# Kernel optimization log

Hardware: AMD Instinct MI355X
Metric: run time of the kernel (lower is better)

The kernel has to match this reference:

```python
import jax, jax.numpy as jnp
import numpy as np
import math

B, SQ, SK, HID, NH = 2, 2048, 512, 1024, 16
HD = HID // NH  # head dim = 64


def setup_inputs() -> dict:
    key = jax.random.key(0)
    k1, k2, k3, k4, k5 = jax.random.split(key, 5)
    return {
        "hidden_states": jax.random.normal(k1, (B, SQ, HID), dtype=jnp.float32),
        "encoder_hidden_states": jax.random.normal(k2, (B, SK, HID), dtype=jnp.float32),
        "encoder_attention_mask": jnp.ones((B, SK), dtype=jnp.int32),
        "Wq": jax.random.normal(k3, (HID, HID), dtype=jnp.float32) * (1.0 / math.sqrt(HID)),
        "Wk": jax.random.normal(k4, (HID, HID), dtype=jnp.float32) * (1.0 / math.sqrt(HID)),
        "Wv": jax.random.normal(k5, (HID, HID), dtype=jnp.float32) * (1.0 / math.sqrt(HID)),
    }


def reference(hidden_states, encoder_hidden_states, encoder_attention_mask, Wq, Wk, Wv):
    # nn.Linear(bias=False): y = x @ W.T ; split heads -> [B, H, S, D]
    def split_heads(x, S):
        return x.reshape(x.shape[0], S, NH, HD).transpose(0, 2, 1, 3)

    q = split_heads(hidden_states @ Wq.T, SQ)            # [B,H,Sq,D]
    k = split_heads(encoder_hidden_states @ Wk.T, SK)    # [B,H,Sk,D]
    v = split_heads(encoder_hidden_states @ Wv.T, SK)    # [B,H,Sk,D]

    scores = jnp.einsum("bhqd,bhkd->bhqk", q, k) / math.sqrt(HD)  # [B,H,Sq,Sk]

    # HF-style extended mask: (1 - mask) * finfo.min, broadcast over heads/queries
    neg = jnp.finfo(scores.dtype).min
    inv_mask = (1.0 - encoder_attention_mask.astype(scores.dtype))[:, None, None, :] * neg

    probs = jax.nn.softmax(scores + inv_mask, axis=-1)
    context = jnp.einsum("bhqk,bhkd->bhqd", probs, v)    # [B,H,Sq,D]
    context = context.transpose(0, 2, 1, 3).reshape(hidden_states.shape[0], SQ, HID)
    # NOTE: returned attention_scores are scaled but UNMASKED, matching the source
    return (context, scores)
```

## Files before the change

kernel.cpp:

```cpp
#include <hip/hip_runtime.h>

#define B_   2
#define SQ_  2048
#define SK_  512
#define HID_ 1024
#define NH_  16
#define HD_  64

typedef __bf16 bf16x8 __attribute__((ext_vector_type(8)));
typedef float  f32x4  __attribute__((ext_vector_type(4)));

__device__ __forceinline__ unsigned short f2bf(float f) {
    unsigned u = __builtin_bit_cast(unsigned, f);
    u += 0x7fffu + ((u >> 16) & 1u);
    return (unsigned short)(u >> 16);
}

__device__ __forceinline__ void gll16(const unsigned short* g, unsigned short* l) {
    __builtin_amdgcn_global_load_lds(
        (const __attribute__((address_space(1))) unsigned int*)(const void*)g,
        (__attribute__((address_space(3))) unsigned int*)(void*)l,
        16, 0, 0);
}

__global__ __launch_bounds__(256) void cvt_all(const float* __restrict__ hs,
                                               const float* __restrict__ enc,
                                               const float* __restrict__ wq,
                                               const float* __restrict__ wk,
                                               const float* __restrict__ wv,
                                               unsigned short* __restrict__ hb,
                                               unsigned short* __restrict__ eb,
                                               unsigned short* __restrict__ wqb,
                                               unsigned short* __restrict__ wkb,
                                               unsigned short* __restrict__ wvb) {
    size_t i = ((size_t)blockIdx.x * 256 + threadIdx.x) * 4;
    const float* s; unsigned short* d; size_t off;
    if (i < 4194304)      { s = hs;  d = hb;  off = i; }
    else if (i < 5242880) { s = enc; d = eb;  off = i - 4194304; }
    else if (i < 6291456) { s = wq;  d = wqb; off = i - 5242880; }
    else if (i < 7340032) { s = wk;  d = wkb; off = i - 6291456; }
    else                  { s = wv;  d = wvb; off = i - 7340032; }
    float4 v = *reinterpret_cast<const float4*>(s + off);
    ushort4 o;
    o.x = f2bf(v.x); o.y = f2bf(v.y); o.z = f2bf(v.z); o.w = f2bf(v.w);
    *reinterpret_cast<ushort4*>(d + off) = o;
}

__global__ __launch_bounds__(256, 4) void gemm_qkv(const unsigned short* __restrict__ hb,
                                                   const unsigned short* __restrict__ eb,
                                                   const unsigned short* __restrict__ wq,
                                                   const unsigned short* __restrict__ wk,
                                                   const unsigned short* __restrict__ wv,
                                                   unsigned short* __restrict__ qo,
                                                   unsigned short* __restrict__ ko,
                                                   unsigned short* __restrict__ vo) {
    __shared__ unsigned short as[64 * 32];
    __shared__ unsigned short bs[128 * 32];

    int bid = blockIdx.x;
    int nb = bid & 7, ms = bid >> 3;
    const unsigned short* Ab; const unsigned short* Wb;
    int mrow, mode;
    if (ms < 64)      { mode = 0; Ab = hb; Wb = wq; mrow = ms * 64; }
    else if (ms < 80) { mode = 1; Ab = eb; Wb = wk; mrow = (ms - 64) * 64; }
    else              { mode = 2; Ab = eb; Wb = wv; mrow = (ms - 80) * 64; }
    int n0 = nb * 128;

    int tid = threadIdx.x, lane = tid & 63, w = tid >> 6;
    int quad = lane >> 4, lc = lane & 15;

    int lrow = lane >> 2;
    int chA  = (lane & 3) ^ ((lane >> 3) & 3);
    const unsigned short* agp  = Ab + (size_t)(mrow + w * 16 + lrow) * 1024 + chA * 8;
    const unsigned short* bgp0 = Wb + (size_t)(n0 + w * 32 + lrow) * 1024 + chA * 8;
    const unsigned short* bgp1 = bgp0 + (size_t)16 * 1024;
    unsigned short* asl  = &as[(w * 16) * 32];
    unsigned short* bsl0 = &bs[(w * 32) * 32];
    unsigned short* bsl1 = &bs[(w * 32 + 16) * 32];

    f32x4 zero4 = {0.f, 0.f, 0.f, 0.f};
    f32x4 acc[4][2];
#pragma unroll
    for (int i = 0; i < 4; i++) { acc[i][0] = zero4; acc[i][1] = zero4; }

    int rsw = (lc >> 1) & 3;
    for (int k0 = 0; k0 < 1024; k0 += 32) {
        gll16(agp + k0, asl);
        gll16(bgp0 + k0, bsl0);
        gll16(bgp1 + k0, bsl1);
        __syncthreads();
        bf16x8 af[4], bfr[2];
#pragma unroll
        for (int mt = 0; mt < 4; mt++)
            af[mt] = *reinterpret_cast<const bf16x8*>(&as[(mt * 16 + lc) * 32 + (quad ^ rsw) * 8]);
#pragma unroll
        for (int nt = 0; nt < 2; nt++)
            bfr[nt] = *reinterpret_cast<const bf16x8*>(&bs[(w * 32 + nt * 16 + lc) * 32 + (quad ^ rsw) * 8]);
#pragma unroll
        for (int mt = 0; mt < 4; mt++)
#pragma unroll
            for (int nt = 0; nt < 2; nt++)
                acc[mt][nt] = __builtin_amdgcn_mfma_f32_16x16x32_bf16(af[mt], bfr[nt], acc[mt][nt], 0, 0, 0);
        __syncthreads();
    }

#pragma unroll
    for (int mt = 0; mt < 4; mt++) {
#pragma unroll
        for (int nt = 0; nt < 2; nt++) {
            int n = n0 + w * 32 + nt * 16 + lc;
            int h = n >> 6, d = n & 63;
#pragma unroll
            for (int r = 0; r < 4; r++) {
                int M = mrow + mt * 16 + quad * 4 + r;
                unsigned short val = f2bf(acc[mt][nt][r]);
                if (mode == 0) {
                    int b = M >> 11, s = M & 2047;
                    qo[(((size_t)(b * NH_ + h)) * SQ_ + s) * HD_ + d] = val;
                } else if (mode == 1) {
                    int b = M >> 9, s = M & 511;
                    ko[(((size_t)(b * NH_ + h)) * SK_ + s) * HD_ + d] = val;
                } else {
                    int b = M >> 9, s = M & 511;
                    vo[(((size_t)(b * NH_ + h)) * HD_ + d) * SK_ + s] = val;
                }
            }
        }
    }
}

#define PST 72

__global__ __launch_bounds__(256, 2) void attn_kernel(const unsigned short* __restrict__ qh,
                                                      const unsigned short* __restrict__ kh,
                                                      const unsigned short* __restrict__ vh,
                                                      const int* __restrict__ maskp,
                                                      float* __restrict__ octx,
                                                      float* __restrict__ oscores) {
    __shared__ unsigned short qs[64 * 64];
    __shared__ unsigned short ks[64 * 64];
    __shared__ unsigned short vts[64 * 64];
    __shared__ unsigned short ps[64 * PST];
    __shared__ float lm[SK_];

    int bid = blockIdx.x;
    int qt = bid & 31;
    int h  = (bid >> 5) & 15;
    int b  = bid >> 9;

    int tid = threadIdx.x, lane = tid & 63, w = tid >> 6;
    int quad = lane >> 4, lc = lane & 15;
    int wrow = w * 16;

    const unsigned short* qp = qh + ((size_t)(b * NH_ + h) * SQ_ + qt * 64) * HD_;
    const unsigned short* kp = kh + ((size_t)(b * NH_ + h) * SK_) * HD_;
    const unsigned short* vp = vh + ((size_t)(b * NH_ + h) * HD_) * SK_;

    int lr  = lane >> 3;
    int chg = (lane & 7) ^ lr;

#pragma unroll
    for (int j = 0; j < 2; j++) {
        int c = w * 2 + j;
        gll16(qp + (c * 8 + lr) * 64 + chg * 8, &qs[c * 512]);
    }
#pragma unroll
    for (int i = 0; i < 2; i++) {
        int c = tid + i * 256;
        lm[c] = maskp[b * SK_ + c] ? 0.0f : -3.0e38f;
    }
    __syncthreads();

    int rsw = lc & 7;
    bf16x8 qf[2];
#pragma unroll
    for (int hf = 0; hf < 2; hf++)
        qf[hf] = *reinterpret_cast<const bf16x8*>(&qs[(wrow + lc) * 64 + ((quad + hf * 4) ^ rsw) * 8]);

    f32x4 zero4 = {0.f, 0.f, 0.f, 0.f};
    f32x4 sacc[32];
#pragma unroll
    for (int t = 0; t < 32; t++) sacc[t] = zero4;

    float* srowp = oscores + ((size_t)(b * NH_ + h) * SQ_ + qt * 64) * SK_;

    for (int kt = 0; kt < 8; kt++) {
#pragma unroll
        for (int j = 0; j < 2; j++) {
            int c = w * 2 + j;
            gll16(kp + (kt * 64 + c * 8 + lr) * 64 + chg * 8, &ks[c * 512]);
        }
        __syncthreads();
#pragma unroll
        for (int tl = 0; tl < 4; tl++) {
            int t = kt * 4 + tl;
#pragma unroll
            for (int hf = 0; hf < 2; hf++) {
                bf16x8 kf = *reinterpret_cast<const bf16x8*>(
                    &ks[(tl * 16 + lc) * 64 + ((quad + hf * 4) ^ rsw) * 8]);
                sacc[t] = __builtin_amdgcn_mfma_f32_16x16x32_bf16(kf, qf[hf], sacc[t], 0, 0, 0);
            }
        }
#pragma unroll
        for (int tl = 0; tl < 4; tl++) {
            int t = kt * 4 + tl;
            sacc[t] *= 0.125f;
            *reinterpret_cast<f32x4*>(&srowp[(size_t)(wrow + lc) * SK_ + t * 16 + quad * 4]) = sacc[t];
        }
        __syncthreads();
    }

#pragma unroll
    for (int t = 0; t < 32; t++) {
        float4 mv = *reinterpret_cast<const float4*>(&lm[t * 16 + quad * 4]);
        sacc[t][0] += mv.x; sacc[t][1] += mv.y; sacc[t][2] += mv.z; sacc[t][3] += mv.w;
    }
    float mx = -3.4e38f;
#pragma unroll
    for (int t = 0; t < 32; t++)
#pragma unroll
        for (int j = 0; j < 4; j++) mx = fmaxf(mx, sacc[t][j]);
    mx = fmaxf(mx, __shfl_xor(mx, 16));
    mx = fmaxf(mx, __shfl_xor(mx, 32));
    float sum = 0.f;
#pragma unroll
    for (int t = 0; t < 32; t++)
#pragma unroll
        for (int j = 0; j < 4; j++) {
            float e = __expf(sacc[t][j] - mx);
            sacc[t][j] = e;
            sum += e;
        }
    sum += __shfl_xor(sum, 16);
    sum += __shfl_xor(sum, 32);
    float inv = 1.0f / sum;
#pragma unroll
    for (int t = 0; t < 32; t++) sacc[t] *= inv;

    f32x4 cacc[4];
#pragma unroll
    for (int ct = 0; ct < 4; ct++) cacc[ct] = zero4;

    for (int kt = 0; kt < 8; kt++) {
#pragma unroll
        for (int tl = 0; tl < 4; tl++) {
            int t = kt * 4 + tl;
            ushort4 pk;
            pk.x = f2bf(sacc[t][0]); pk.y = f2bf(sacc[t][1]);
            pk.z = f2bf(sacc[t][2]); pk.w = f2bf(sacc[t][3]);
            *reinterpret_cast<ushort4*>(&ps[(wrow + lc) * PST + tl * 16 + quad * 4]) = pk;
        }
#pragma unroll
        for (int j = 0; j < 2; j++) {
            int c = w * 2 + j;
            gll16(vp + (size_t)(c * 8 + lr) * SK_ + kt * 64 + chg * 8, &vts[c * 512]);
        }
        __syncthreads();
#pragma unroll
        for (int ks2 = 0; ks2 < 2; ks2++) {
            bf16x8 af = *reinterpret_cast<const bf16x8*>(&ps[(wrow + lc) * PST + ks2 * 32 + quad * 8]);
#pragma unroll
            for (int ct = 0; ct < 4; ct++) {
                bf16x8 bv = *reinterpret_cast<const bf16x8*>(
                    &vts[(ct * 16 + lc) * 64 + ((quad + ks2 * 4) ^ rsw) * 8]);
                cacc[ct] = __builtin_amdgcn_mfma_f32_16x16x32_bf16(af, bv, cacc[ct], 0, 0, 0);
            }
        }
        __syncthreads();
    }

#pragma unroll
    for (int ct = 0; ct < 4; ct++) {
        int d = ct * 16 + lc;
#pragma unroll
        for (int r = 0; r < 4; r++) {
            int s = qt * 64 + wrow + quad * 4 + r;
            octx[((size_t)b * SQ_ + s) * HID_ + h * HD_ + d] = cacc[ct][r];
        }
    }
}

extern "C" void kernel_launch(void* const* d_in, const int* in_sizes, int n_in,
                              void* d_out, int out_size, void* d_ws, size_t ws_size,
                              hipStream_t stream) {
    const float* hs   = (const float*)d_in[0];
    const float* enc  = (const float*)d_in[1];
    const int*   mask = (const int*)d_in[2];
    const float* Wq   = (const float*)d_in[3];
    const float* Wk   = (const float*)d_in[4];
    const float* Wv   = (const float*)d_in[5];
    float* out = (float*)d_out;

    unsigned short* hb  = (unsigned short*)d_ws;
    unsigned short* eb  = hb  + 4194304;
    unsigned short* wqb = eb  + 1048576;
    unsigned short* wkb = wqb + 1048576;
    unsigned short* wvb = wkb + 1048576;
    unsigned short* qhp = wvb + 1048576;
    unsigned short* khp = qhp + 4194304;
    unsigned short* vhp = khp + 1048576;

    cvt_all<<<8192, 256, 0, stream>>>(hs, enc, Wq, Wk, Wv, hb, eb, wqb, wkb, wvb);
    gemm_qkv<<<768, 256, 0, stream>>>(hb, eb, wqb, wkb, wvb, qhp, khp, vhp);
    attn_kernel<<<1024, 256, 0, stream>>>(qhp, khp, vhp, mask, out, out + 4194304);
}
```

Measured before the change: 228.3 us.

## Enlarge QKV GEMM tiles to 128x128, load K/V fragments directly from global memory

The QKV GEMM now uses 128x128 output tiles with a 2x2 warp grid and 16 accumulators per wave. This halves the block count and raises operand reuse per LDS load. Both kernels remap block IDs so each group of 8 consecutive blocks touches different tiles, likely for better cache or XCD locality. The attention kernel drops its LDS staging for Q, K and V, reading MFMA fragments straight from global memory and removing the per-iteration barriers. This relies on L1/L2 reuse across waves, at the cost of uncoalesced reads and higher register pressure.

```diff
diff --git a/kernel.cpp b/kernel.cpp
--- a/kernel.cpp
+++ b/kernel.cpp
@@ -46,7 +46,7 @@
     *reinterpret_cast<ushort4*>(d + off) = o;
 }
 
-__global__ __launch_bounds__(256, 4) void gemm_qkv(const unsigned short* __restrict__ hb,
+__global__ __launch_bounds__(256, 3) void gemm_qkv(const unsigned short* __restrict__ hb,
                                                    const unsigned short* __restrict__ eb,
                                                    const unsigned short* __restrict__ wq,
                                                    const unsigned short* __restrict__ wk,
@@ -54,52 +54,61 @@
                                                    unsigned short* __restrict__ qo,
                                                    unsigned short* __restrict__ ko,
                                                    unsigned short* __restrict__ vo) {
-    __shared__ unsigned short as[64 * 32];
+    __shared__ unsigned short as[128 * 32];
     __shared__ unsigned short bs[128 * 32];
 
     int bid = blockIdx.x;
+    bid = (bid & 7) * 48 + (bid >> 3);
     int nb = bid & 7, ms = bid >> 3;
     const unsigned short* Ab; const unsigned short* Wb;
     int mrow, mode;
-    if (ms < 64)      { mode = 0; Ab = hb; Wb = wq; mrow = ms * 64; }
-    else if (ms < 80) { mode = 1; Ab = eb; Wb = wk; mrow = (ms - 64) * 64; }
-    else              { mode = 2; Ab = eb; Wb = wv; mrow = (ms - 80) * 64; }
+    if (ms < 32)      { mode = 0; Ab = hb; Wb = wq; mrow = ms * 128; }
+    else if (ms < 40) { mode = 1; Ab = eb; Wb = wk; mrow = (ms - 32) * 128; }
+    else              { mode = 2; Ab = eb; Wb = wv; mrow = (ms - 40) * 128; }
     int n0 = nb * 128;
 
     int tid = threadIdx.x, lane = tid & 63, w = tid >> 6;
     int quad = lane >> 4, lc = lane & 15;
+    int wr = w >> 1, wc = w & 1;
 
     int lrow = lane >> 2;
     int chA  = (lane & 3) ^ ((lane >> 3) & 3);
-    const unsigned short* agp  = Ab + (size_t)(mrow + w * 16 + lrow) * 1024 + chA * 8;
+    const unsigned short* agp0 = Ab + (size_t)(mrow + w * 32 + lrow) * 1024 + chA * 8;
+    const unsigned short* agp1 = agp0 + (size_t)16 * 1024;
     const unsigned short* bgp0 = Wb + (size_t)(n0 + w * 32 + lrow) * 1024 + chA * 8;
     const unsigned short* bgp1 = bgp0 + (size_t)16 * 1024;
-    unsigned short* asl  = &as[(w * 16) * 32];
+    unsigned short* asl0 = &as[(w * 32) * 32];
+    unsigned short* asl1 = &as[(w * 32 + 16) * 32];
     unsigned short* bsl0 = &bs[(w * 32) * 32];
     unsigned short* bsl1 = &bs[(w * 32 + 16) * 32];
 
     f32x4 zero4 = {0.f, 0.f, 0.f, 0.f};
-    f32x4 acc[4][2];
-#pragma unroll
-    for (int i = 0; i < 4; i++) { acc[i][0] = zero4; acc[i][1] = zero4; }
+    f32x4 acc[4][4];
+#pragma unroll
+    for (int i = 0; i < 4; i++)
+#pragma unroll
+        for (int j = 0; j < 4; j++) acc[i][j] = zero4;
 
     int rsw = (lc >> 1) & 3;
     for (int k0 = 0; k0 < 1024; k0 += 32) {
-        gll16(agp + k0, asl);
+        gll16(agp0 + k0, asl0);
+        gll16(agp1 + k0, asl1);
         gll16(bgp0 + k0, bsl0);
         gll16(bgp1 + k0, bsl1);
         __syncthreads();
-        bf16x8 af[4], bfr[2];
+        bf16x8 af[4], bfr[4];
 #pragma unroll
         for (int mt = 0; mt < 4; mt++)
-            af[mt] = *reinterpret_cast<const bf16x8*>(&as[(mt * 16 + lc) * 32 + (quad ^ rsw) * 8]);
-#pragma unroll
-        for (int nt = 0; nt < 2; nt++)
-            bfr[nt] = *reinterpret_cast<const bf16x8*>(&bs[(w * 32 + nt * 16 + lc) * 32 + (quad ^ rsw) * 8]);
+            af[mt] = *reinterpret_cast<const bf16x8*>(
+                &as[(wr * 64 + mt * 16 + lc) * 32 + (quad ^ rsw) * 8]);
+#pragma unroll
+        for (int nt = 0; nt < 4; nt++)
+            bfr[nt] = *reinterpret_cast<const bf16x8*>(
+                &bs[(wc * 64 + nt * 16 + lc) * 32 + (quad ^ rsw) * 8]);
 #pragma unroll
         for (int mt = 0; mt < 4; mt++)
 #pragma unroll
-            for (int nt = 0; nt < 2; nt++)
+            for (int nt = 0; nt < 4; nt++)
                 acc[mt][nt] = __builtin_amdgcn_mfma_f32_16x16x32_bf16(af[mt], bfr[nt], acc[mt][nt], 0, 0, 0);
         __syncthreads();
     }
@@ -107,12 +116,12 @@
 #pragma unroll
     for (int mt = 0; mt < 4; mt++) {
 #pragma unroll
-        for (int nt = 0; nt < 2; nt++) {
-            int n = n0 + w * 32 + nt * 16 + lc;
+        for (int nt = 0; nt < 4; nt++) {
+            int n = n0 + wc * 64 + nt * 16 + lc;
             int h = n >> 6, d = n & 63;
 #pragma unroll
             for (int r = 0; r < 4; r++) {
-                int M = mrow + mt * 16 + quad * 4 + r;
+                int M = mrow + wr * 64 + mt * 16 + quad * 4 + r;
                 unsigned short val = f2bf(acc[mt][nt][r]);
                 if (mode == 0) {
                     int b = M >> 11, s = M & 2047;
@@ -137,13 +146,11 @@
                                                       const int* __restrict__ maskp,
                                                       float* __restrict__ octx,
                                                       float* __restrict__ oscores) {
-    __shared__ unsigned short qs[64 * 64];
-    __shared__ unsigned short ks[64 * 64];
-    __shared__ unsigned short vts[64 * 64];
     __shared__ unsigned short ps[64 * PST];
     __shared__ float lm[SK_];
 
     int bid = blockIdx.x;
+    bid = (bid & 7) * 128 + (bid >> 3);
     int qt = bid & 31;
     int h  = (bid >> 5) & 15;
     int b  = bid >> 9;
@@ -156,14 +163,6 @@
     const unsigned short* kp = kh + ((size_t)(b * NH_ + h) * SK_) * HD_;
     const unsigned short* vp = vh + ((size_t)(b * NH_ + h) * HD_) * SK_;
 
-    int lr  = lane >> 3;
-    int chg = (lane & 7) ^ lr;
-
-#pragma unroll
-    for (int j = 0; j < 2; j++) {
-        int c = w * 2 + j;
-        gll16(qp + (c * 8 + lr) * 64 + chg * 8, &qs[c * 512]);
-    }
 #pragma unroll
     for (int i = 0; i < 2; i++) {
         int c = tid + i * 256;
@@ -171,11 +170,10 @@
     }
     __syncthreads();
 
-    int rsw = lc & 7;
     bf16x8 qf[2];
 #pragma unroll
     for (int hf = 0; hf < 2; hf++)
-        qf[hf] = *reinterpret_cast<const bf16x8*>(&qs[(wrow + lc) * 64 + ((quad + hf * 4) ^ rsw) * 8]);
+        qf[hf] = *reinterpret_cast<const bf16x8*>(qp + (wrow + lc) * 64 + hf * 32 + quad * 8);
 
     f32x4 zero4 = {0.f, 0.f, 0.f, 0.f};
     f32x4 sacc[32];
@@ -184,20 +182,15 @@
 
     float* srowp = oscores + ((size_t)(b * NH_ + h) * SQ_ + qt * 64) * SK_;
 
+#pragma unroll
     for (int kt = 0; kt < 8; kt++) {
-#pragma unroll
-        for (int j = 0; j < 2; j++) {
-            int c = w * 2 + j;
-            gll16(kp + (kt * 64 + c * 8 + lr) * 64 + chg * 8, &ks[c * 512]);
-        }
-        __syncthreads();
 #pragma unroll
         for (int tl = 0; tl < 4; tl++) {
             int t = kt * 4 + tl;
+            const unsigned short* krow = kp + (kt * 64 + tl * 16 + lc) * 64 + quad * 8;
 #pragma unroll
             for (int hf = 0; hf < 2; hf++) {
-                bf16x8 kf = *reinterpret_cast<const bf16x8*>(
-                    &ks[(tl * 16 + lc) * 64 + ((quad + hf * 4) ^ rsw) * 8]);
+                bf16x8 kf = *reinterpret_cast<const bf16x8*>(krow + hf * 32);
                 sacc[t] = __builtin_amdgcn_mfma_f32_16x16x32_bf16(kf, qf[hf], sacc[t], 0, 0, 0);
             }
         }
@@ -207,7 +200,6 @@
             sacc[t] *= 0.125f;
             *reinterpret_cast<f32x4*>(&srowp[(size_t)(wrow + lc) * SK_ + t * 16 + quad * 4]) = sacc[t];
         }
-        __syncthreads();
     }
 
 #pragma unroll
@@ -241,6 +233,7 @@
 #pragma unroll
     for (int ct = 0; ct < 4; ct++) cacc[ct] = zero4;
 
+#pragma unroll
     for (int kt = 0; kt < 8; kt++) {
 #pragma unroll
         for (int tl = 0; tl < 4; tl++) {
@@ -251,22 +244,15 @@
             *reinterpret_cast<ushort4*>(&ps[(wrow + lc) * PST + tl * 16 + quad * 4]) = pk;
         }
 #pragma unroll
-        for (int j = 0; j < 2; j++) {
-            int c = w * 2 + j;
-            gll16(vp + (size_t)(c * 8 + lr) * SK_ + kt * 64 + chg * 8, &vts[c * 512]);
-        }
-        __syncthreads();
-#pragma unroll
         for (int ks2 = 0; ks2 < 2; ks2++) {
             bf16x8 af = *reinterpret_cast<const bf16x8*>(&ps[(wrow + lc) * PST + ks2 * 32 + quad * 8]);
 #pragma unroll
             for (int ct = 0; ct < 4; ct++) {
                 bf16x8 bv = *reinterpret_cast<const bf16x8*>(
-                    &vts[(ct * 16 + lc) * 64 + ((quad + ks2 * 4) ^ rsw) * 8]);
+                    vp + (size_t)(ct * 16 + lc) * SK_ + kt * 64 + ks2 * 32 + quad * 8);
                 cacc[ct] = __builtin_amdgcn_mfma_f32_16x16x32_bf16(af, bv, cacc[ct], 0, 0, 0);
             }
         }
-        __syncthreads();
     }
 
 #pragma unroll
@@ -301,6 +287,6 @@
     unsigned short* vhp = khp + 1048576;
 
     cvt_all<<<8192, 256, 0, stream>>>(hs, enc, Wq, Wk, Wv, hb, eb, wqb, wkb, wvb);
-    gemm_qkv<<<768, 256, 0, stream>>>(hb, eb, wqb, wkb, wvb, qhp, khp, vhp);
+    gemm_qkv<<<384, 256, 0, stream>>>(hb, eb, wqb, wkb, wvb, qhp, khp, vhp);
     attn_kernel<<<1024, 256, 0, stream>>>(qhp, khp, vhp, mask, out, out + 4194304);
 }
```

Measured after the change: 268.3 us. +17.5%, slower.

## Double-buffer LDS tiles in QKV GEMM and attention, remap blocks across XCDs

Applied to the files above, without the earlier changes.

Both the projection GEMM and the attention kernel now double-buffer their LDS tiles (A/W tiles, K tiles, V^T tiles). The next tile's global-to-LDS load is issued before computing on the current one, and one barrier per iteration is dropped, so load latency is meant to overlap with MFMA work. Block indices are permuted with a stride-8 remap so neighbouring logical tiles land on the same XCD, aiming for better L2 reuse of shared weights and K/V. The scaled score stores move out of the QK loop into one pass after it. The cost is roughly double the LDS use, which could cut occupancy, and correctness now depends on the end-of-iteration barrier waiting for the outstanding async loads.

```diff
diff --git a/kernel.cpp b/kernel.cpp
--- a/kernel.cpp
+++ b/kernel.cpp
@@ -54,10 +54,11 @@
                                                    unsigned short* __restrict__ qo,
                                                    unsigned short* __restrict__ ko,
                                                    unsigned short* __restrict__ vo) {
-    __shared__ unsigned short as[64 * 32];
-    __shared__ unsigned short bs[128 * 32];
+    __shared__ unsigned short as[2][64 * 32];
+    __shared__ unsigned short bs[2][128 * 32];
 
     int bid = blockIdx.x;
+    bid = (bid & 7) * 96 + (bid >> 3);
     int nb = bid & 7, ms = bid >> 3;
     const unsigned short* Ab; const unsigned short* Wb;
     int mrow, mode;
@@ -74,9 +75,6 @@
     const unsigned short* agp  = Ab + (size_t)(mrow + w * 16 + lrow) * 1024 + chA * 8;
     const unsigned short* bgp0 = Wb + (size_t)(n0 + w * 32 + lrow) * 1024 + chA * 8;
     const unsigned short* bgp1 = bgp0 + (size_t)16 * 1024;
-    unsigned short* asl  = &as[(w * 16) * 32];
-    unsigned short* bsl0 = &bs[(w * 32) * 32];
-    unsigned short* bsl1 = &bs[(w * 32 + 16) * 32];
 
     f32x4 zero4 = {0.f, 0.f, 0.f, 0.f};
     f32x4 acc[4][2];
@@ -84,18 +82,28 @@
     for (int i = 0; i < 4; i++) { acc[i][0] = zero4; acc[i][1] = zero4; }
 
     int rsw = (lc >> 1) & 3;
-    for (int k0 = 0; k0 < 1024; k0 += 32) {
-        gll16(agp + k0, asl);
-        gll16(bgp0 + k0, bsl0);
-        gll16(bgp1 + k0, bsl1);
-        __syncthreads();
+
+    gll16(agp,  &as[0][(w * 16) * 32]);
+    gll16(bgp0, &bs[0][(w * 32) * 32]);
+    gll16(bgp1, &bs[0][(w * 32 + 16) * 32]);
+    __syncthreads();
+
+#pragma unroll 2
+    for (int it = 0; it < 32; ++it) {
+        int cur = it & 1;
+        if (it < 31) {
+            int k0n = (it + 1) * 32;
+            gll16(agp + k0n,  &as[cur ^ 1][(w * 16) * 32]);
+            gll16(bgp0 + k0n, &bs[cur ^ 1][(w * 32) * 32]);
+            gll16(bgp1 + k0n, &bs[cur ^ 1][(w * 32 + 16) * 32]);
+        }
         bf16x8 af[4], bfr[2];
 #pragma unroll
         for (int mt = 0; mt < 4; mt++)
-            af[mt] = *reinterpret_cast<const bf16x8*>(&as[(mt * 16 + lc) * 32 + (quad ^ rsw) * 8]);
+            af[mt] = *reinterpret_cast<const bf16x8*>(&as[cur][(mt * 16 + lc) * 32 + (quad ^ rsw) * 8]);
 #pragma unroll
         for (int nt = 0; nt < 2; nt++)
-            bfr[nt] = *reinterpret_cast<const bf16x8*>(&bs[(w * 32 + nt * 16 + lc) * 32 + (quad ^ rsw) * 8]);
+            bfr[nt] = *reinterpret_cast<const bf16x8*>(&bs[cur][(w * 32 + nt * 16 + lc) * 32 + (quad ^ rsw) * 8]);
 #pragma unroll
         for (int mt = 0; mt < 4; mt++)
 #pragma unroll
@@ -138,12 +146,13 @@
                                                       float* __restrict__ octx,
                                                       float* __restrict__ oscores) {
     __shared__ unsigned short qs[64 * 64];
-    __shared__ unsigned short ks[64 * 64];
-    __shared__ unsigned short vts[64 * 64];
+    __shared__ unsigned short ks[2][64 * 64];
+    __shared__ unsigned short vts[2][64 * 64];
     __shared__ unsigned short ps[64 * PST];
     __shared__ float lm[SK_];
 
     int bid = blockIdx.x;
+    bid = (bid & 7) * 128 + (bid >> 3);
     int qt = bid & 31;
     int h  = (bid >> 5) & 15;
     int b  = bid >> 9;
@@ -163,6 +172,7 @@
     for (int j = 0; j < 2; j++) {
         int c = w * 2 + j;
         gll16(qp + (c * 8 + lr) * 64 + chg * 8, &qs[c * 512]);
+        gll16(kp + (c * 8 + lr) * 64 + chg * 8, &ks[0][c * 512]);
     }
 #pragma unroll
     for (int i = 0; i < 2; i++) {
@@ -182,32 +192,41 @@
 #pragma unroll
     for (int t = 0; t < 32; t++) sacc[t] = zero4;
 
-    float* srowp = oscores + ((size_t)(b * NH_ + h) * SQ_ + qt * 64) * SK_;
-
+#pragma unroll
     for (int kt = 0; kt < 8; kt++) {
-#pragma unroll
-        for (int j = 0; j < 2; j++) {
-            int c = w * 2 + j;
-            gll16(kp + (kt * 64 + c * 8 + lr) * 64 + chg * 8, &ks[c * 512]);
-        }
-        __syncthreads();
+        const unsigned short* kcur = ks[kt & 1];
+        if (kt < 7) {
+            unsigned short* knxt = ks[(kt + 1) & 1];
+#pragma unroll
+            for (int j = 0; j < 2; j++) {
+                int c = w * 2 + j;
+                gll16(kp + ((kt + 1) * 64 + c * 8 + lr) * 64 + chg * 8, &knxt[c * 512]);
+            }
+        }
 #pragma unroll
         for (int tl = 0; tl < 4; tl++) {
             int t = kt * 4 + tl;
 #pragma unroll
             for (int hf = 0; hf < 2; hf++) {
                 bf16x8 kf = *reinterpret_cast<const bf16x8*>(
-                    &ks[(tl * 16 + lc) * 64 + ((quad + hf * 4) ^ rsw) * 8]);
+                    &kcur[(tl * 16 + lc) * 64 + ((quad + hf * 4) ^ rsw) * 8]);
                 sacc[t] = __builtin_amdgcn_mfma_f32_16x16x32_bf16(kf, qf[hf], sacc[t], 0, 0, 0);
             }
         }
-#pragma unroll
-        for (int tl = 0; tl < 4; tl++) {
-            int t = kt * 4 + tl;
-            sacc[t] *= 0.125f;
-            *reinterpret_cast<f32x4*>(&srowp[(size_t)(wrow + lc) * SK_ + t * 16 + quad * 4]) = sacc[t];
-        }
         __syncthreads();
+    }
+
+    float* srowp = oscores + ((size_t)(b * NH_ + h) * SQ_ + qt * 64) * SK_;
+#pragma unroll
+    for (int t = 0; t < 32; t++) {
+        sacc[t] *= 0.125f;
+        *reinterpret_cast<f32x4*>(&srowp[(size_t)(wrow + lc) * SK_ + t * 16 + quad * 4]) = sacc[t];
+    }
+
+#pragma unroll
+    for (int j = 0; j < 2; j++) {
+        int c = w * 2 + j;
+        gll16(vp + (size_t)(c * 8 + lr) * SK_ + chg * 8, &vts[0][c * 512]);
     }
 
 #pragma unroll
@@ -237,11 +256,23 @@
 #pragma unroll
     for (int t = 0; t < 32; t++) sacc[t] *= inv;
 
+    __syncthreads();
+
     f32x4 cacc[4];
 #pragma unroll
     for (int ct = 0; ct < 4; ct++) cacc[ct] = zero4;
 
+#pragma unroll
     for (int kt = 0; kt < 8; kt++) {
+        const unsigned short* vcur = vts[kt & 1];
+        if (kt < 7) {
+            unsigned short* vnxt = vts[(kt + 1) & 1];
+#pragma unroll
+            for (int j = 0; j < 2; j++) {
+                int c = w * 2 + j;
+                gll16(vp + (size_t)(c * 8 + lr) * SK_ + (kt + 1) * 64 + chg * 8, &vnxt[c * 512]);
+            }
+        }
 #pragma unroll
         for (int tl = 0; tl < 4; tl++) {
             int t = kt * 4 + tl;
@@ -251,18 +282,12 @@
             *reinterpret_cast<ushort4*>(&ps[(wrow + lc) * PST + tl * 16 + quad * 4]) = pk;
         }
 #pragma unroll
-        for (int j = 0; j < 2; j++) {
-            int c = w * 2 + j;
-            gll16(vp + (size_t)(c * 8 + lr) * SK_ + kt * 64 + chg * 8, &vts[c * 512]);
-        }
-        __syncthreads();
-#pragma unroll
         for (int ks2 = 0; ks2 < 2; ks2++) {
             bf16x8 af = *reinterpret_cast<const bf16x8*>(&ps[(wrow + lc) * PST + ks2 * 32 + quad * 8]);
 #pragma unroll
             for (int ct = 0; ct < 4; ct++) {
                 bf16x8 bv = *reinterpret_cast<const bf16x8*>(
-                    &vts[(ct * 16 + lc) * 64 + ((quad + ks2 * 4) ^ rsw) * 8]);
+                    &vcur[(ct * 16 + lc) * 64 + ((quad + ks2 * 4) ^ rsw) * 8]);
                 cacc[ct] = __builtin_amdgcn_mfma_f32_16x16x32_bf16(af, bv, cacc[ct], 0, 0, 0);
             }
         }
```

New measurement: 229.7 us. Within noise of the previous version (+0.6%).
